# Performance work log

Measured on AMD Instinct MI355X. Metric: run time of the kernel, lower is better.

## Reference

```python
import jax, jax.numpy as jnp
import numpy as np

N = 100000      # total nodes (herb + ingredient + target concatenated)
E = 1600000     # edges (all etypes concatenated)
D_IN = 128
D_HID = 128
D_OUT = 128
BN_EPS = 1e-5
LEAKY_SLOPE = 0.01


def setup_inputs() -> dict:
    key = jax.random.key(0)
    ks = jax.random.split(key, 8)
    x = jax.random.normal(ks[0], (N, D_IN), dtype=jnp.float32)
    src = jax.random.randint(ks[1], (E,), 0, N, dtype=jnp.int32)
    dst = jax.random.randint(ks[2], (E,), 0, N, dtype=jnp.int32)
    W1 = jax.random.normal(ks[3], (D_IN, D_HID), dtype=jnp.float32) * (1.0 / np.sqrt(D_IN))
    b1 = jnp.zeros((D_HID,), jnp.float32)
    W2 = jax.random.normal(ks[4], (D_HID, D_OUT), dtype=jnp.float32) * (1.0 / np.sqrt(D_HID))
    b2 = jnp.zeros((D_OUT,), jnp.float32)
    gamma = jnp.ones((D_HID,), jnp.float32)
    beta = jnp.zeros((D_HID,), jnp.float32)
    run_mean = jax.random.normal(ks[5], (D_HID,), jnp.float32) * 0.1
    run_var = jax.random.uniform(ks[6], (D_HID,), jnp.float32, 0.5, 1.5)
    return {"x": x, "src": src, "dst": dst, "W1": W1, "b1": b1,
            "W2": W2, "b2": b2, "gamma": gamma, "beta": beta,
            "run_mean": run_mean, "run_var": run_var}


def _graph_conv(h, s, d, W, b, norm_src, norm_dst):
    # DGL GraphConv, norm='both': D_out^{-1/2} then sum-aggregate then D_in^{-1/2}, then linear
    h = h * norm_src                                   # [N, d]
    m = jax.ops.segment_sum(h[s], d, num_segments=N)   # gather + spmm-aggregate
    m = m * norm_dst
    return m @ W + b


def reference(x, src, dst, W1, b1, W2, b2, gamma, beta, run_mean, run_var):
    # dgl.add_self_loop: append (i, i) for every node
    loop = jnp.arange(N, dtype=src.dtype)
    s = jnp.concatenate([src, loop])
    d = jnp.concatenate([dst, loop])
    ones = jnp.ones(s.shape[0], jnp.float32)
    out_deg = jnp.maximum(jax.ops.segment_sum(ones, s, num_segments=N), 1.0)
    in_deg = jnp.maximum(jax.ops.segment_sum(ones, d, num_segments=N), 1.0)
    norm_src = (out_deg ** -0.5)[:, None]
    norm_dst = (in_deg ** -0.5)[:, None]

    # layer 0: conv -> BN (eval, running stats) -> leaky_relu -> dropout (eval = identity)
    h = _graph_conv(x, s, d, W1, b1, norm_src, norm_dst)
    h = (h - run_mean) * jax.lax.rsqrt(run_var + BN_EPS) * gamma + beta
    h = jnp.where(h > 0, h, LEAKY_SLOPE * h)

    # layer 1 (last): conv only
    h = _graph_conv(h, s, d, W2, b2, norm_src, norm_dst)
    return h
```

## Files before the change

kernel.cpp:

```cpp
#include <hip/hip_runtime.h>

#define NN 100000
#define NE 1600000
#define D 128
#define LEAKY 0.01f
#define BNEPS 1e-5f

#define G 256
#define CHUNK 6250
#define B 782
#define BSHIFT 7
#define BMASK 127

typedef short v8s __attribute__((ext_vector_type(8)));
typedef float v4f __attribute__((ext_vector_type(4)));

__device__ __forceinline__ unsigned f2bf(float f) {
    unsigned u = __float_as_uint(f);
    return (u + 0x7fffu + ((u >> 16) & 1u)) >> 16;
}
__device__ __forceinline__ float bf2f(unsigned h) {
    return __uint_as_float(h << 16);
}


__global__ __launch_bounds__(256) void hist_kernel(const int* __restrict__ src,
                                                   const int* __restrict__ dst,
                                                   int* __restrict__ deg,
                                                   int* __restrict__ hist) {
    __shared__ int h[B];
    for (int i = threadIdx.x; i < B; i += 256) h[i] = 0;
    __syncthreads();
    int g = blockIdx.x;
    const int* dp = dst + g * CHUNK;
    const int* sp = src + g * CHUNK;
    for (int k = threadIdx.x; k < CHUNK; k += 256) {
        atomicAdd(&h[dp[k] >> BSHIFT], 1);
        atomicAdd(&deg[sp[k]], 1);
    }
    __syncthreads();
    for (int i = threadIdx.x; i < B; i += 256) hist[i * G + g] = h[i];
}

__global__ void scanA(const int* __restrict__ a, int* __restrict__ bsum) {
    __shared__ int sm[256];
    int t = threadIdx.x;
    sm[t] = a[blockIdx.x * 256 + t];
    __syncthreads();
    for (int s = 128; s > 0; s >>= 1) {
        if (t < s) sm[t] += sm[t + s];
        __syncthreads();
    }
    if (t == 0) bsum[blockIdx.x] = sm[0];
}

__global__ void scanB(const int* __restrict__ bsum, int* __restrict__ boffs) {
    int lane = threadIdx.x;
    int run = 0;
    for (int base = 0; base < B; base += 64) {
        int i = base + lane;
        int v = (i < B) ? bsum[i] : 0;
        int orig = v;
        for (int off = 1; off < 64; off <<= 1) {
            int t = __shfl_up(v, off);
            if (lane >= off) v += t;
        }
        if (i < B) boffs[i] = run + v - orig;
        run += __shfl(v, 63);
    }
}

__global__ void scanC(const int* __restrict__ a, const int* __restrict__ boffs,
                      int* __restrict__ offs) {
    __shared__ int sm[256];
    int t = threadIdx.x;
    int i = blockIdx.x * 256 + t;
    int v = a[i];
    sm[t] = v;
    __syncthreads();
    for (int off = 1; off < 256; off <<= 1) {
        int x = (t >= off) ? sm[t - off] : 0;
        __syncthreads();
        sm[t] += x;
        __syncthreads();
    }
    offs[i] = boffs[blockIdx.x] + sm[t] - v;
}

__global__ __launch_bounds__(256) void sort_kernel(const int* __restrict__ src,
                                                   const int* __restrict__ dst,
                                                   const int* __restrict__ offs,
                                                   unsigned* __restrict__ ebuf) {
    __shared__ int cur[B];
    int g = blockIdx.x;
    for (int i = threadIdx.x; i < B; i += 256) cur[i] = offs[i * G + g];
    __syncthreads();
    const int* sp = src + g * CHUNK;
    const int* dp = dst + g * CHUNK;
    for (int k = threadIdx.x; k < CHUNK; k += 256) {
        int d = dp[k], s = sp[k];
        int pos = atomicAdd(&cur[d >> BSHIFT], 1);
        ebuf[pos] = ((unsigned)(d & BMASK) << 17) | (unsigned)s;
    }
}


__global__ __launch_bounds__(256) void conv_kernel(const float* __restrict__ x,
                                                   const int* __restrict__ deg,
                                                   float* __restrict__ norm_s,
                                                   unsigned* __restrict__ hb) {
    int t = blockIdx.x * 256 + threadIdx.x;
    if (t >= NN * 64) return;
    int row = t >> 6;
    float ns = rsqrtf((float)(deg[row] + 1));
    if ((t & 63) == 0) norm_s[row] = ns;
    float2 v = ((const float2*)x)[t];
    hb[t] = f2bf(v.x * ns) | (f2bf(v.y * ns) << 16);
}


__global__ __launch_bounds__(256) void local_sort(
    const int* __restrict__ offs, unsigned* __restrict__ ebuf,
    int* __restrict__ row, float* __restrict__ norm_d)
{
    __shared__ int cnt[128];
    __shared__ int sc[128];
    const int b = blockIdx.x;
    const int t = threadIdx.x;
    const int s = offs[b * G];
    const int e = (b == B - 1) ? NE : offs[(b + 1) * G];
    if (t < 128) cnt[t] = 0;
    __syncthreads();

    unsigned ent[16];
    int nent = 0;
    for (int k = s + t; k < e && nent < 16; k += 256) {
        unsigned u = ebuf[k];
        ent[nent++] = u;
        atomicAdd(&cnt[u >> 17], 1);
    }
    __syncthreads();

    if (t < 128) sc[t] = cnt[t];
    __syncthreads();
    for (int off = 1; off < 128; off <<= 1) {
        int v = 0;
        if (t < 128 && t >= off) v = sc[t - off];
        __syncthreads();
        if (t < 128) sc[t] += v;
        __syncthreads();
    }
    if (t < 128) {
        int st = s + sc[t] - cnt[t];
        int node = b * 128 + t;
        if (node < NN) {
            row[node] = st;
            norm_d[node] = rsqrtf((float)(cnt[t] + 1));
        }
        cnt[t] = st;
    }
    if (b == B - 1 && t == 0) row[NN] = NE;
    __syncthreads();

    for (int i = 0; i < nent; ++i) {
        unsigned u = ent[i];
        int pos = atomicAdd(&cnt[u >> 17], 1);
        ebuf[pos] = u & 0x1FFFFu;
    }
}


__global__ __launch_bounds__(256) void csr_agg(
    const int* __restrict__ row, const int* __restrict__ csr,
    const unsigned* __restrict__ hp,
    unsigned* __restrict__ Ahi, unsigned* __restrict__ Alo)
{
    int i = blockIdx.x * 4 + (threadIdx.x >> 6);
    if (i >= NN) return;
    int lane = threadIdx.x & 63;

    float2 acc;
    {
        unsigned u = hp[(size_t)i * 64 + lane];
        acc.x = __uint_as_float(u << 16);
        acc.y = __uint_as_float(u & 0xffff0000u);
    }

    int start = row[i], end = row[i + 1];
    for (int base = start; base < end; base += 64) {
        int n = end - base; if (n > 64) n = 64;
        int sv = csr[base + (lane < n ? lane : n - 1)];
        int j = 0;
        for (; j + 8 <= n; j += 8) {
            int ss[8]; unsigned uu[8];
            #pragma unroll
            for (int t = 0; t < 8; ++t) ss[t] = __shfl(sv, j + t);
            #pragma unroll
            for (int t = 0; t < 8; ++t) uu[t] = hp[(size_t)ss[t] * 64 + lane];
            #pragma unroll
            for (int t = 0; t < 8; ++t) {
                acc.x += __uint_as_float(uu[t] << 16);
                acc.y += __uint_as_float(uu[t] & 0xffff0000u);
            }
        }
        for (; j < n; ++j) {
            int s = __shfl(sv, j);
            unsigned u = hp[(size_t)s * 64 + lane];
            acc.x += __uint_as_float(u << 16);
            acc.y += __uint_as_float(u & 0xffff0000u);
        }
    }
    unsigned hx = f2bf(acc.x), hy = f2bf(acc.y);
    float lx = acc.x - bf2f(hx), ly = acc.y - bf2f(hy);
    Ahi[(size_t)i * 64 + lane] = hx | (hy << 16);
    Alo[(size_t)i * 64 + lane] = f2bf(lx) | (f2bf(ly) << 16);
}


template<bool LAYER0>
__global__ __launch_bounds__(256) void gemm_kernel(
    const unsigned* __restrict__ Ahi_g, const unsigned* __restrict__ Alo_g,
    const float* __restrict__ W, const float* __restrict__ bias,
    const float* __restrict__ norm_s, const float* __restrict__ norm_d,
    const float* __restrict__ gamma, const float* __restrict__ beta,
    const float* __restrict__ rmean, const float* __restrict__ rvar,
    float* __restrict__ outf, unsigned short* __restrict__ outb)
{
    __shared__ unsigned lhi[64 * 68];
    __shared__ unsigned llo[64 * 68];

    const int w    = threadIdx.x >> 6;
    const int lane = threadIdx.x & 63;
    const int quad = lane >> 4;
    const int l16  = lane & 15;

    v8s Bhi[2][4], Blo[2][4];
    int col[2];
    #pragma unroll
    for (int ct = 0; ct < 2; ++ct) {
        col[ct] = 32 * w + 16 * ct + l16;
        #pragma unroll
        for (int q = 0; q < 4; ++q) {
            int kb = 32 * q + quad * 8;
            v8s hi8, lo8;
            #pragma unroll
            for (int kk = 0; kk < 8; ++kk) {
                float wv = W[(kb + kk) * D + col[ct]];
                unsigned h = f2bf(wv);
                hi8[kk] = (short)h;
                lo8[kk] = (short)f2bf(wv - bf2f(h));
            }
            Bhi[ct][q] = hi8;
            Blo[ct][q] = lo8;
        }
    }

    float bcol[2], s[2] = {0.f, 0.f}, sh[2] = {0.f, 0.f};
    #pragma unroll
    for (int ct = 0; ct < 2; ++ct) {
        bcol[ct] = bias[col[ct]];
        if (LAYER0) {
            s[ct]  = gamma[col[ct]] * rsqrtf(rvar[col[ct]] + BNEPS);
            sh[ct] = beta[col[ct]] - rmean[col[ct]] * s[ct];
        }
    }

    for (int row0 = blockIdx.x * 64; row0 < NN; row0 += gridDim.x * 64) {
        __syncthreads();
        for (int idx = threadIdx.x; idx < 64 * 64; idx += 256) {
            int r = idx >> 6, cp = idx & 63;
            int rw = row0 + r;
            unsigned vh = 0, vl = 0;
            if (rw < NN) {
                vh = Ahi_g[(size_t)rw * 64 + cp];
                vl = Alo_g[(size_t)rw * 64 + cp];
            }
            lhi[r * 68 + cp] = vh;
            llo[r * 68 + cp] = vl;
        }
        __syncthreads();

        #pragma unroll
        for (int rt = 0; rt < 4; ++rt) {
            v4f acc0 = {0.f, 0.f, 0.f, 0.f};
            v4f acc1 = {0.f, 0.f, 0.f, 0.f};
            #pragma unroll
            for (int q = 0; q < 4; ++q) {
                const unsigned short* ph = (const unsigned short*)lhi
                    + (rt * 16 + l16) * 136 + q * 32 + quad * 8;
                const unsigned short* pl = (const unsigned short*)llo
                    + (rt * 16 + l16) * 136 + q * 32 + quad * 8;
                v8s ahi = *(const v8s*)ph;
                v8s alo = *(const v8s*)pl;
                acc0 = __builtin_amdgcn_mfma_f32_16x16x32_bf16(ahi, Bhi[0][q], acc0, 0, 0, 0);
                acc0 = __builtin_amdgcn_mfma_f32_16x16x32_bf16(alo, Bhi[0][q], acc0, 0, 0, 0);
                acc0 = __builtin_amdgcn_mfma_f32_16x16x32_bf16(ahi, Blo[0][q], acc0, 0, 0, 0);
                acc1 = __builtin_amdgcn_mfma_f32_16x16x32_bf16(ahi, Bhi[1][q], acc1, 0, 0, 0);
                acc1 = __builtin_amdgcn_mfma_f32_16x16x32_bf16(alo, Bhi[1][q], acc1, 0, 0, 0);
                acc1 = __builtin_amdgcn_mfma_f32_16x16x32_bf16(ahi, Blo[1][q], acc1, 0, 0, 0);
            }
            #pragma unroll
            for (int r = 0; r < 4; ++r) {
                int rw = row0 + rt * 16 + quad * 4 + r;
                if (rw >= NN) continue;
                float nd = norm_d[rw];
                float o0 = acc0[r] * nd + bcol[0];
                float o1 = acc1[r] * nd + bcol[1];
                if (LAYER0) {
                    o0 = o0 * s[0] + sh[0];
                    o1 = o1 * s[1] + sh[1];
                    o0 = o0 > 0.f ? o0 : LEAKY * o0;
                    o1 = o1 > 0.f ? o1 : LEAKY * o1;
                    float ns = norm_s[rw];
                    o0 *= ns; o1 *= ns;
                    outb[(size_t)rw * D + col[0]] = (unsigned short)f2bf(o0);
                    outb[(size_t)rw * D + col[1]] = (unsigned short)f2bf(o1);
                } else {
                    outf[(size_t)rw * D + col[0]] = o0;
                    outf[(size_t)rw * D + col[1]] = o1;
                }
            }
        }
    }
}


extern "C" void kernel_launch(void* const* d_in, const int* in_sizes, int n_in,
                              void* d_out, int out_size, void* d_ws, size_t ws_size,
                              hipStream_t stream) {
    const float* x     = (const float*)d_in[0];
    const int*   src   = (const int*)d_in[1];
    const int*   dst   = (const int*)d_in[2];
    const float* W1    = (const float*)d_in[3];
    const float* b1    = (const float*)d_in[4];
    const float* W2    = (const float*)d_in[5];
    const float* b2    = (const float*)d_in[6];
    const float* gamma = (const float*)d_in[7];
    const float* beta  = (const float*)d_in[8];
    const float* rmean = (const float*)d_in[9];
    const float* rvar  = (const float*)d_in[10];
    float* out = (float*)d_out;

    unsigned* hb = (unsigned*)d_out;

    unsigned* Ahi   = (unsigned*)d_ws;
    unsigned* Alo   = Ahi + (size_t)NN * 64;
    float*    norm  = (float*)(Alo + (size_t)NN * 64);
    int*      deg   = (int*)(norm + 2 * NN);
    int*      hist  = deg + NN;
    int*      offs  = hist + B * G;
    int*      bsum  = offs + B * G;
    int*      boffs = bsum + B;
    unsigned* ebuf  = (unsigned*)(boffs + B);
    float* norm_s = norm;
    float* norm_d = norm + NN;
    int*   row    = hist;

    hipMemsetAsync(deg, 0, NN * sizeof(int), stream);

    hist_kernel<<<G, 256, 0, stream>>>(src, dst, deg, hist);
    scanA<<<B * G / 256, 256, 0, stream>>>(hist, bsum);
    scanB<<<1, 64, 0, stream>>>(bsum, boffs);
    scanC<<<B * G / 256, 256, 0, stream>>>(hist, boffs, offs);
    sort_kernel<<<G, 256, 0, stream>>>(src, dst, offs, ebuf);
    conv_kernel<<<(NN * 64 + 255) / 256, 256, 0, stream>>>(x, deg, norm_s, hb);
    local_sort<<<B, 256, 0, stream>>>(offs, ebuf, row, norm_d);

    const int AGG_BLOCKS = (NN + 3) / 4;
    const int GEMM_BLOCKS = 784;
    csr_agg<<<AGG_BLOCKS, 256, 0, stream>>>(row, (const int*)ebuf, hb, Ahi, Alo);
    gemm_kernel<true><<<GEMM_BLOCKS, 256, 0, stream>>>(Ahi, Alo, W1, b1,
                                                       norm_s, norm_d,
                                                       gamma, beta, rmean, rvar,
                                                       nullptr, (unsigned short*)hb);
    csr_agg<<<AGG_BLOCKS, 256, 0, stream>>>(row, (const int*)ebuf, hb, Ahi, Alo);
    gemm_kernel<false><<<GEMM_BLOCKS, 256, 0, stream>>>(Ahi, Alo, W2, b2,
                                                        norm_s, norm_d,
                                                        nullptr, nullptr, nullptr, nullptr,
                                                        out, nullptr);
}
```

Baseline: 456.2 us.

## Replace global-atomic out-degree count with bucketed sort, widen aggregation loads

Out-degree counting no longer uses global atomics per edge. Sources are bucketed by a second histogram, scan and scatter pass, then counted with shared-memory atomics per bucket. Histogram and sort kernels move to 1024-thread blocks. csr_agg now splits each wavefront into two halves that each gather a different edge with 8-byte loads, then combines the halves with a cross-lane xor shuffle. The cost is three extra scan launches, an extra scatter buffer, and more bookkeeping traffic.

After: 436.0 us. 4.4% less time.

```diff
diff --git a/kernel.cpp b/kernel.cpp
--- a/kernel.cpp
+++ b/kernel.cpp
@@ -24,22 +24,26 @@
 }
 
 
-__global__ __launch_bounds__(256) void hist_kernel(const int* __restrict__ src,
-                                                   const int* __restrict__ dst,
-                                                   int* __restrict__ deg,
-                                                   int* __restrict__ hist) {
+__global__ __launch_bounds__(1024) void hist_kernel(const int* __restrict__ src,
+                                                    const int* __restrict__ dst,
+                                                    int* __restrict__ hist,
+                                                    int* __restrict__ hist2) {
     __shared__ int h[B];
-    for (int i = threadIdx.x; i < B; i += 256) h[i] = 0;
+    __shared__ int h2[B];
+    for (int i = threadIdx.x; i < B; i += 1024) { h[i] = 0; h2[i] = 0; }
     __syncthreads();
     int g = blockIdx.x;
     const int* dp = dst + g * CHUNK;
     const int* sp = src + g * CHUNK;
-    for (int k = threadIdx.x; k < CHUNK; k += 256) {
+    for (int k = threadIdx.x; k < CHUNK; k += 1024) {
         atomicAdd(&h[dp[k] >> BSHIFT], 1);
-        atomicAdd(&deg[sp[k]], 1);
-    }
-    __syncthreads();
-    for (int i = threadIdx.x; i < B; i += 256) hist[i * G + g] = h[i];
+        atomicAdd(&h2[sp[k] >> BSHIFT], 1);
+    }
+    __syncthreads();
+    for (int i = threadIdx.x; i < B; i += 1024) {
+        hist[i * G + g]  = h[i];
+        hist2[i * G + g] = h2[i];
+    }
 }
 
 __global__ void scanA(const int* __restrict__ a, int* __restrict__ bsum) {
@@ -87,20 +91,47 @@
     offs[i] = boffs[blockIdx.x] + sm[t] - v;
 }
 
-__global__ __launch_bounds__(256) void sort_kernel(const int* __restrict__ src,
-                                                   const int* __restrict__ dst,
-                                                   const int* __restrict__ offs,
-                                                   unsigned* __restrict__ ebuf) {
+__global__ __launch_bounds__(1024) void sort_kernel(const int* __restrict__ src,
+                                                    const int* __restrict__ dst,
+                                                    const int* __restrict__ offs,
+                                                    const int* __restrict__ offs2,
+                                                    unsigned* __restrict__ ebuf,
+                                                    unsigned* __restrict__ sbuf) {
     __shared__ int cur[B];
+    __shared__ int cur2[B];
     int g = blockIdx.x;
-    for (int i = threadIdx.x; i < B; i += 256) cur[i] = offs[i * G + g];
+    for (int i = threadIdx.x; i < B; i += 1024) {
+        cur[i]  = offs[i * G + g];
+        cur2[i] = offs2[i * G + g];
+    }
     __syncthreads();
     const int* sp = src + g * CHUNK;
     const int* dp = dst + g * CHUNK;
-    for (int k = threadIdx.x; k < CHUNK; k += 256) {
+    for (int k = threadIdx.x; k < CHUNK; k += 1024) {
         int d = dp[k], s = sp[k];
         int pos = atomicAdd(&cur[d >> BSHIFT], 1);
         ebuf[pos] = ((unsigned)(d & BMASK) << 17) | (unsigned)s;
+        int pos2 = atomicAdd(&cur2[s >> BSHIFT], 1);
+        sbuf[pos2] = (unsigned)s;
+    }
+}
+
+__global__ __launch_bounds__(256) void deg_count(const int* __restrict__ offs2,
+                                                 const unsigned* __restrict__ sbuf,
+                                                 int* __restrict__ deg) {
+    __shared__ int cnt[128];
+    const int b = blockIdx.x;
+    const int t = threadIdx.x;
+    const int s = offs2[b * G];
+    const int e = (b == B - 1) ? NE : offs2[(b + 1) * G];
+    if (t < 128) cnt[t] = 0;
+    __syncthreads();
+    for (int k = s + t; k < e; k += 256)
+        atomicAdd(&cnt[sbuf[k] & BMASK], 1);
+    __syncthreads();
+    if (t < 128) {
+        int node = b * 128 + t;
+        if (node < NN) deg[node] = cnt[t];
     }
 }
 
@@ -171,49 +202,74 @@
 
 
 __global__ __launch_bounds__(256) void csr_agg(
-    const int* __restrict__ row, const int* __restrict__ csr,
+    const int* __restrict__ rowp, const int* __restrict__ csr,
     const unsigned* __restrict__ hp,
     unsigned* __restrict__ Ahi, unsigned* __restrict__ Alo)
 {
     int i = blockIdx.x * 4 + (threadIdx.x >> 6);
     if (i >= NN) return;
-    int lane = threadIdx.x & 63;
-
-    float2 acc;
-    {
-        unsigned u = hp[(size_t)i * 64 + lane];
-        acc.x = __uint_as_float(u << 16);
-        acc.y = __uint_as_float(u & 0xffff0000u);
-    }
-
-    int start = row[i], end = row[i + 1];
+    const int lane = threadIdx.x & 63;
+    const int half = lane >> 5;
+    const int c2   = lane & 31;
+
+    float4 acc = {0.f, 0.f, 0.f, 0.f};
+    if (half == 0) {
+        uint2 u = *(const uint2*)(hp + (size_t)i * 64 + 2 * c2);
+        acc.x = __uint_as_float(u.x << 16);
+        acc.y = __uint_as_float(u.x & 0xffff0000u);
+        acc.z = __uint_as_float(u.y << 16);
+        acc.w = __uint_as_float(u.y & 0xffff0000u);
+    }
+
+    int start = rowp[i], end = rowp[i + 1];
     for (int base = start; base < end; base += 64) {
         int n = end - base; if (n > 64) n = 64;
         int sv = csr[base + (lane < n ? lane : n - 1)];
         int j = 0;
-        for (; j + 8 <= n; j += 8) {
-            int ss[8]; unsigned uu[8];
-            #pragma unroll
-            for (int t = 0; t < 8; ++t) ss[t] = __shfl(sv, j + t);
-            #pragma unroll
-            for (int t = 0; t < 8; ++t) uu[t] = hp[(size_t)ss[t] * 64 + lane];
+        for (; j + 16 <= n; j += 16) {
+            int ss[8]; uint2 uu[8];
+            #pragma unroll
+            for (int t = 0; t < 8; ++t) ss[t] = __shfl(sv, j + 2 * t + half);
+            #pragma unroll
+            for (int t = 0; t < 8; ++t)
+                uu[t] = *(const uint2*)(hp + (size_t)ss[t] * 64 + 2 * c2);
             #pragma unroll
             for (int t = 0; t < 8; ++t) {
-                acc.x += __uint_as_float(uu[t] << 16);
-                acc.y += __uint_as_float(uu[t] & 0xffff0000u);
-            }
-        }
-        for (; j < n; ++j) {
-            int s = __shfl(sv, j);
-            unsigned u = hp[(size_t)s * 64 + lane];
-            acc.x += __uint_as_float(u << 16);
-            acc.y += __uint_as_float(u & 0xffff0000u);
-        }
-    }
-    unsigned hx = f2bf(acc.x), hy = f2bf(acc.y);
-    float lx = acc.x - bf2f(hx), ly = acc.y - bf2f(hy);
-    Ahi[(size_t)i * 64 + lane] = hx | (hy << 16);
-    Alo[(size_t)i * 64 + lane] = f2bf(lx) | (f2bf(ly) << 16);
+                acc.x += __uint_as_float(uu[t].x << 16);
+                acc.y += __uint_as_float(uu[t].x & 0xffff0000u);
+                acc.z += __uint_as_float(uu[t].y << 16);
+                acc.w += __uint_as_float(uu[t].y & 0xffff0000u);
+            }
+        }
+        for (; j < n; j += 2) {
+            int e = j + half;
+            int sidx = __shfl(sv, e < n ? e : n - 1);
+            if (e < n) {
+                uint2 u2 = *(const uint2*)(hp + (size_t)sidx * 64 + 2 * c2);
+                acc.x += __uint_as_float(u2.x << 16);
+                acc.y += __uint_as_float(u2.x & 0xffff0000u);
+                acc.z += __uint_as_float(u2.y << 16);
+                acc.w += __uint_as_float(u2.y & 0xffff0000u);
+            }
+        }
+    }
+
+    acc.x += __shfl_xor(acc.x, 32);
+    acc.y += __shfl_xor(acc.y, 32);
+    acc.z += __shfl_xor(acc.z, 32);
+    acc.w += __shfl_xor(acc.w, 32);
+
+    unsigned h0 = f2bf(acc.x), h1 = f2bf(acc.y);
+    unsigned h2 = f2bf(acc.z), h3 = f2bf(acc.w);
+    if (half == 0) {
+        uint2 w = { h0 | (h1 << 16), h2 | (h3 << 16) };
+        *(uint2*)(Ahi + (size_t)i * 64 + 2 * c2) = w;
+    } else {
+        float l0 = acc.x - bf2f(h0), l1 = acc.y - bf2f(h1);
+        float l2 = acc.z - bf2f(h2), l3 = acc.w - bf2f(h3);
+        uint2 w = { f2bf(l0) | (f2bf(l1) << 16), f2bf(l2) | (f2bf(l3) << 16) };
+        *(uint2*)(Alo + (size_t)i * 64 + 2 * c2) = w;
+    }
 }
 
 
@@ -356,13 +412,19 @@
     float* norm_d = norm + NN;
     int*   row    = hist;
 
-    hipMemsetAsync(deg, 0, NN * sizeof(int), stream);
-
-    hist_kernel<<<G, 256, 0, stream>>>(src, dst, deg, hist);
+    int*      hist2 = (int*)Ahi;
+    int*      offs2 = hist2 + B * G;
+    unsigned* sbuf  = (unsigned*)(offs2 + B * G);
+
+    hist_kernel<<<G, 1024, 0, stream>>>(src, dst, hist, hist2);
     scanA<<<B * G / 256, 256, 0, stream>>>(hist, bsum);
     scanB<<<1, 64, 0, stream>>>(bsum, boffs);
     scanC<<<B * G / 256, 256, 0, stream>>>(hist, boffs, offs);
-    sort_kernel<<<G, 256, 0, stream>>>(src, dst, offs, ebuf);
+    scanA<<<B * G / 256, 256, 0, stream>>>(hist2, bsum);
+    scanB<<<1, 64, 0, stream>>>(bsum, boffs);
+    scanC<<<B * G / 256, 256, 0, stream>>>(hist2, boffs, offs2);
+    sort_kernel<<<G, 1024, 0, stream>>>(src, dst, offs, offs2, ebuf, sbuf);
+    deg_count<<<B, 256, 0, stream>>>(offs2, sbuf, deg);
     conv_kernel<<<(NN * 64 + 255) / 256, 256, 0, stream>>>(x, deg, norm_s, hb);
     local_sort<<<B, 256, 0, stream>>>(offs, ebuf, row, norm_d);
 
```
